# Kernel optimization log

Hardware: AMD Instinct MI355X
Metric: run time of the kernel (lower is better)

Reference implementation:

```python
import jax, jax.numpy as jnp
import numpy as np

WINDOW_SIZES = (4, 8, 16)
STRIDE_FACTOR = 0.5
EPS = 1e-6


def _pool_scale(x, mask_f, w, stride):
    # x: [B,T,D], mask_f: [B,T] float. Overlapping masked mean via prefix sums.
    B, T, D = x.shape
    xm = x * mask_f[:, :, None]
    cx = jnp.concatenate([jnp.zeros((B, 1, D), x.dtype), jnp.cumsum(xm, axis=1)], axis=1)  # [B,T+1,D]
    cm = jnp.concatenate([jnp.zeros((B, 1), x.dtype), jnp.cumsum(mask_f, axis=1)], axis=1)  # [B,T+1]
    starts = jnp.arange(0, T - w + 1, stride)  # [S]
    num = cx[:, starts + w, :] - cx[:, starts, :]          # [B,S,D] masked window sums
    valid = cm[:, starts + w] - cm[:, starts]              # [B,S] valid counts
    avg = num / jnp.clip(valid, EPS)[:, :, None]
    return avg, valid > 0


def setup_inputs() -> dict:
    key = jax.random.key(0)
    k1, k2 = jax.random.split(key)
    B, T, D = 8, 4096, 512
    x = jax.random.normal(k1, (B, T, D), dtype=jnp.float32)
    mask = jax.random.bernoulli(k2, 0.9, (B, T))  # bool, True=valid
    return {"x": x, "mask": mask}


def reference(x, mask):
    mask_f = mask.astype(x.dtype)
    vis_list, msk_list = [], []
    for w in WINDOW_SIZES:
        stride = max(1, int(w * STRIDE_FACTOR))
        avg, m = _pool_scale(x, mask_f, w, stride)
        vis_list.append(avg)
        msk_list.append(m)
    return (*vis_list, *msk_list)
```

## Files before the change

kernel.cpp:

```cpp
#include <hip/hip_runtime.h>


#define EPS 1e-6f

typedef float f4 __attribute__((ext_vector_type(4)));

constexpr int B = 8, T = 4096, D = 512, D4 = D / 4;
constexpr int TILE = 32;
constexpr int HALO = 8;
constexpr int NT = TILE + HALO;
constexpr int NP = NT / 2;
constexpr int NTILES = T / TILE;
constexpr int S4 = 2047, S8 = 1023, S16 = 511;

constexpr size_t OFF0 = 0;
constexpr size_t OFF1 = (size_t)B * S4 * D;
constexpr size_t OFF2 = OFF1 + (size_t)B * S8 * D;
constexpr size_t OFF3 = OFF2 + (size_t)B * S16 * D;
constexpr size_t OFF4 = OFF3 + (size_t)B * S4;
constexpr size_t OFF5 = OFF4 + (size_t)B * S8;

template <bool GUARD>
__device__ __forceinline__ void tile_body(const f4* __restrict__ x4,
                                          const int* __restrict__ mask,
                                          float* __restrict__ out, int b,
                                          int tile, int d4, int lane,
                                          bool write_masks) {
  const int t0 = tile * TILE;

  const int* mp = mask + (size_t)b * T + t0;
  float mf[NT];
#pragma unroll
  for (int i = 0; i < NT; ++i) {
    int m = (!GUARD || (t0 + i) < T) ? mp[i] : 0;
    mf[i] = (m != 0) ? 1.0f : 0.0f;
  }

  float c2[NP];
#pragma unroll
  for (int i = 0; i < NP; ++i) c2[i] = mf[2 * i] + mf[2 * i + 1];
  float c4[19];
#pragma unroll
  for (int j = 0; j < 19; ++j) c4[j] = c2[j] + c2[j + 1];
  float c8[9];
#pragma unroll
  for (int k = 0; k < 9; ++k) c8[k] = c4[2 * k] + c4[2 * k + 2];
  float c16[4];
#pragma unroll
  for (int l = 0; l < 4; ++l) c16[l] = c8[2 * l] + c8[2 * l + 2];

  float i4[16], i8[8], i16[4];
#pragma unroll
  for (int j = 0; j < 16; ++j) i4[j] = 1.0f / fmaxf(c4[j], EPS);
#pragma unroll
  for (int k = 0; k < 8; ++k) i8[k] = 1.0f / fmaxf(c8[k], EPS);
#pragma unroll
  for (int l = 0; l < 4; ++l) i16[l] = 1.0f / fmaxf(c16[l], EPS);

  if (write_masks) {
    if (lane < 16) {
      int s = tile * 16 + lane;
      if (!GUARD || s < S4) {
        float c = 0.f;
#pragma unroll
        for (int j = 0; j < 16; ++j) c = (lane == j) ? c4[j] : c;
        out[OFF3 + (size_t)b * S4 + s] = (c > 0.f) ? 1.f : 0.f;
      }
    } else if (lane < 24) {
      int k = lane - 16, s = tile * 8 + k;
      if (!GUARD || s < S8) {
        float c = 0.f;
#pragma unroll
        for (int j = 0; j < 8; ++j) c = (k == j) ? c8[j] : c;
        out[OFF4 + (size_t)b * S8 + s] = (c > 0.f) ? 1.f : 0.f;
      }
    } else if (lane < 28) {
      int l = lane - 24, s = tile * 4 + l;
      if (!GUARD || s < S16) {
        float c = 0.f;
#pragma unroll
        for (int j = 0; j < 4; ++j) c = (l == j) ? c16[j] : c;
        out[OFF5 + (size_t)b * S16 + s] = (c > 0.f) ? 1.f : 0.f;
      }
    }
  }

  const f4* xb = x4 + (size_t)b * T * D4 + d4;
  f4 p[NP];
#pragma unroll
  for (int i = 0; i < NP; ++i) {
    int t = t0 + 2 * i;
    f4 a0 = {0.f, 0.f, 0.f, 0.f}, a1 = {0.f, 0.f, 0.f, 0.f};
    if (!GUARD || t < T) {
      a0 = xb[(size_t)t * D4];
      a1 = xb[(size_t)(t + 1) * D4];
    }
    p[i] = a0 * mf[2 * i] + a1 * mf[2 * i + 1];
  }

  f4 q4[19];
#pragma unroll
  for (int j = 0; j < 19; ++j) q4[j] = p[j] + p[j + 1];
  f4 q8[9];
#pragma unroll
  for (int k = 0; k < 9; ++k) q8[k] = q4[2 * k] + q4[2 * k + 2];

  f4* o4 = (f4*)(out + OFF0) + ((size_t)b * S4 + (size_t)tile * 16) * D4 + d4;
#pragma unroll
  for (int j = 0; j < 16; ++j) {
    if (!GUARD || (tile * 16 + j) < S4) {
      f4 v = q4[j] * i4[j];
      __builtin_nontemporal_store(v, o4 + (size_t)j * D4);
    }
  }

  f4* o8 = (f4*)(out + OFF1) + ((size_t)b * S8 + (size_t)tile * 8) * D4 + d4;
#pragma unroll
  for (int k = 0; k < 8; ++k) {
    if (!GUARD || (tile * 8 + k) < S8) {
      f4 v = q8[k] * i8[k];
      __builtin_nontemporal_store(v, o8 + (size_t)k * D4);
    }
  }

  f4* o16 = (f4*)(out + OFF2) + ((size_t)b * S16 + (size_t)tile * 4) * D4 + d4;
#pragma unroll
  for (int l = 0; l < 4; ++l) {
    if (!GUARD || (tile * 4 + l) < S16) {
      f4 v = (q8[2 * l] + q8[2 * l + 2]) * i16[l];
      __builtin_nontemporal_store(v, o16 + (size_t)l * D4);
    }
  }
}

__global__ __launch_bounds__(64)
void tpp_kernel(const f4* __restrict__ x4, const int* __restrict__ mask,
                float* __restrict__ out) {
  const int lane = threadIdx.x;
  const int d4 = blockIdx.x * 64 + lane;
  const int b = blockIdx.z;
  const int tile = blockIdx.y;
  const bool write_masks = (blockIdx.x == 0);

  if (tile < NTILES - 1)
    tile_body<false>(x4, mask, out, b, tile, d4, lane, write_masks);
  else
    tile_body<true>(x4, mask, out, b, tile, d4, lane, write_masks);
}

extern "C" void kernel_launch(void* const* d_in, const int* in_sizes, int n_in,
                              void* d_out, int out_size, void* d_ws,
                              size_t ws_size, hipStream_t stream) {
  const f4* x4 = (const f4*)d_in[0];
  const int* mask = (const int*)d_in[1];
  float* out = (float*)d_out;
  dim3 grid(D4 / 64, NTILES, B);
  tpp_kernel<<<grid, 64, 0, stream>>>(x4, mask, out);
}
```

Measured before the change: 109.2 us.

## Narrow per-thread vectors to float2, interleave size-4 stores, use hardware reciprocal

Each thread now handles a float2 instead of a float4 slice of D, which doubles the grid along D and roughly halves per-thread register use. The size-4 window outputs are stored as soon as they are computed, and only the even partial sums are kept, so fewer vectors stay live. Division is replaced with the hardware rcp approximation, and launch bounds now ask for 4 waves per EU. In exchange, each load and store is narrower (8 bytes instead of 16), more blocks run, and the mask and count arithmetic is repeated in twice as many threads.

```diff
diff --git a/kernel.cpp b/kernel.cpp
--- a/kernel.cpp
+++ b/kernel.cpp
@@ -3,9 +3,9 @@
 
 #define EPS 1e-6f
 
-typedef float f4 __attribute__((ext_vector_type(4)));
+typedef float f2 __attribute__((ext_vector_type(2)));
 
-constexpr int B = 8, T = 4096, D = 512, D4 = D / 4;
+constexpr int B = 8, T = 4096, D = 512, D2 = D / 2;
 constexpr int TILE = 32;
 constexpr int HALO = 8;
 constexpr int NT = TILE + HALO;
@@ -21,10 +21,10 @@
 constexpr size_t OFF5 = OFF4 + (size_t)B * S8;
 
 template <bool GUARD>
-__device__ __forceinline__ void tile_body(const f4* __restrict__ x4,
+__device__ __forceinline__ void tile_body(const f2* __restrict__ x2,
                                           const int* __restrict__ mask,
                                           float* __restrict__ out, int b,
-                                          int tile, int d4, int lane,
+                                          int tile, int d2, int lane,
                                           bool write_masks) {
   const int t0 = tile * TILE;
 
@@ -51,11 +51,11 @@
 
   float i4[16], i8[8], i16[4];
 #pragma unroll
-  for (int j = 0; j < 16; ++j) i4[j] = 1.0f / fmaxf(c4[j], EPS);
+  for (int j = 0; j < 16; ++j) i4[j] = __builtin_amdgcn_rcpf(fmaxf(c4[j], EPS));
 #pragma unroll
-  for (int k = 0; k < 8; ++k) i8[k] = 1.0f / fmaxf(c8[k], EPS);
+  for (int k = 0; k < 8; ++k) i8[k] = __builtin_amdgcn_rcpf(fmaxf(c8[k], EPS));
 #pragma unroll
-  for (int l = 0; l < 4; ++l) i16[l] = 1.0f / fmaxf(c16[l], EPS);
+  for (int l = 0; l < 4; ++l) i16[l] = __builtin_amdgcn_rcpf(fmaxf(c16[l], EPS));
 
   if (write_masks) {
     if (lane < 16) {
@@ -85,75 +85,77 @@
     }
   }
 
-  const f4* xb = x4 + (size_t)b * T * D4 + d4;
-  f4 p[NP];
+  const f2* xb = x2 + (size_t)b * T * D2 + d2;
+  f2 p[NP];
 #pragma unroll
   for (int i = 0; i < NP; ++i) {
     int t = t0 + 2 * i;
-    f4 a0 = {0.f, 0.f, 0.f, 0.f}, a1 = {0.f, 0.f, 0.f, 0.f};
+    f2 a0 = {0.f, 0.f}, a1 = {0.f, 0.f};
     if (!GUARD || t < T) {
-      a0 = xb[(size_t)t * D4];
-      a1 = xb[(size_t)(t + 1) * D4];
+      a0 = xb[(size_t)t * D2];
+      a1 = xb[(size_t)(t + 1) * D2];
     }
     p[i] = a0 * mf[2 * i] + a1 * mf[2 * i + 1];
   }
 
-  f4 q4[19];
+  f2* o4 = (f2*)(out + OFF0) + ((size_t)b * S4 + (size_t)tile * 16) * D2 + d2;
+  f2 q4e[10];
 #pragma unroll
-  for (int j = 0; j < 19; ++j) q4[j] = p[j] + p[j + 1];
-  f4 q8[9];
+  for (int j = 0; j < 19; ++j) {
+    f2 q = p[j] + p[j + 1];
+    if (j < 16) {
+      if (!GUARD || (tile * 16 + j) < S4) {
+        f2 v = q * i4[j];
+        __builtin_nontemporal_store(v, o4 + (size_t)j * D2);
+      }
+    }
+    if ((j & 1) == 0) q4e[j >> 1] = q;
+  }
+
+  f2 q8[9];
 #pragma unroll
-  for (int k = 0; k < 9; ++k) q8[k] = q4[2 * k] + q4[2 * k + 2];
+  for (int k = 0; k < 9; ++k) q8[k] = q4e[k] + q4e[k + 1];
 
-  f4* o4 = (f4*)(out + OFF0) + ((size_t)b * S4 + (size_t)tile * 16) * D4 + d4;
+  f2* o8 = (f2*)(out + OFF1) + ((size_t)b * S8 + (size_t)tile * 8) * D2 + d2;
 #pragma unroll
-  for (int j = 0; j < 16; ++j) {
-    if (!GUARD || (tile * 16 + j) < S4) {
-      f4 v = q4[j] * i4[j];
-      __builtin_nontemporal_store(v, o4 + (size_t)j * D4);
+  for (int k = 0; k < 8; ++k) {
+    if (!GUARD || (tile * 8 + k) < S8) {
+      f2 v = q8[k] * i8[k];
+      __builtin_nontemporal_store(v, o8 + (size_t)k * D2);
     }
   }
 
-  f4* o8 = (f4*)(out + OFF1) + ((size_t)b * S8 + (size_t)tile * 8) * D4 + d4;
-#pragma unroll
-  for (int k = 0; k < 8; ++k) {
-    if (!GUARD || (tile * 8 + k) < S8) {
-      f4 v = q8[k] * i8[k];
-      __builtin_nontemporal_store(v, o8 + (size_t)k * D4);
-    }
-  }
-
-  f4* o16 = (f4*)(out + OFF2) + ((size_t)b * S16 + (size_t)tile * 4) * D4 + d4;
+  f2* o16 = (f2*)(out + OFF2) + ((size_t)b * S16 + (size_t)tile * 4) * D2 + d2;
 #pragma unroll
   for (int l = 0; l < 4; ++l) {
     if (!GUARD || (tile * 4 + l) < S16) {
-      f4 v = (q8[2 * l] + q8[2 * l + 2]) * i16[l];
-      __builtin_nontemporal_store(v, o16 + (size_t)l * D4);
+      f2 v = (q8[2 * l] + q8[2 * l + 2]) * i16[l];
+      __builtin_nontemporal_store(v, o16 + (size_t)l * D2);
     }
   }
 }
 
-__global__ __launch_bounds__(64)
-void tpp_kernel(const f4* __restrict__ x4, const int* __restrict__ mask,
+__global__ __launch_bounds__(64, 4)
+void tpp_kernel(const f2* __restrict__ x2, const int* __restrict__ mask,
                 float* __restrict__ out) {
   const int lane = threadIdx.x;
-  const int d4 = blockIdx.x * 64 + lane;
+  const int d2 = blockIdx.x * 64 + lane;
   const int b = blockIdx.z;
   const int tile = blockIdx.y;
   const bool write_masks = (blockIdx.x == 0);
 
   if (tile < NTILES - 1)
-    tile_body<false>(x4, mask, out, b, tile, d4, lane, write_masks);
+    tile_body<false>(x2, mask, out, b, tile, d2, lane, write_masks);
   else
-    tile_body<true>(x4, mask, out, b, tile, d4, lane, write_masks);
+    tile_body<true>(x2, mask, out, b, tile, d2, lane, write_masks);
 }
 
 extern "C" void kernel_launch(void* const* d_in, const int* in_sizes, int n_in,
                               void* d_out, int out_size, void* d_ws,
                               size_t ws_size, hipStream_t stream) {
-  const f4* x4 = (const f4*)d_in[0];
+  const f2* x2 = (const f2*)d_in[0];
   const int* mask = (const int*)d_in[1];
   float* out = (float*)d_out;
-  dim3 grid(D4 / 64, NTILES, B);
-  tpp_kernel<<<grid, 64, 0, stream>>>(x4, mask, out);
+  dim3 grid(D2 / 64, NTILES, B);
+  tpp_kernel<<<grid, 64, 0, stream>>>(x2, mask, out);
 }
```

Result: slower. 114.0 us (+4.4%).
